# Kernel optimization log

Measured on AMD Instinct MI355X. Metric: run time of the kernel, lower is better.

Reference implementation:

```python
import jax, jax.numpy as jnp
import numpy as np

BN_EPS = 1e-5

def _square_distance(src, dst):
    # src [B,N,3], dst [B,S,3] -> [B,N,S]
    d = -2.0 * jnp.einsum('bnc,bsc->bns', src, dst)
    d = d + jnp.sum(src * src, -1)[:, :, None]
    d = d + jnp.sum(dst * dst, -1)[:, None, :]
    return d

def _conv_bn_relu(x, w, b, g, beta):
    # x [B,C,N]; 1x1 conv == channel GEMM, then training-mode batchnorm over (B,N)
    y = jnp.einsum('oc,bcn->bon', w, x) + b[None, :, None]
    mean = jnp.mean(y, axis=(0, 2), keepdims=True)
    var = jnp.mean((y - mean) ** 2, axis=(0, 2), keepdims=True)  # biased, as torch BN uses for normalization
    y = (y - mean) * jax.lax.rsqrt(var + BN_EPS)
    y = y * g[None, :, None] + beta[None, :, None]
    return jax.nn.relu(y)

def setup_inputs() -> dict:
    key = jax.random.key(0)
    ks = jax.random.split(key, 8)
    B, N, S, D1, D2 = 8, 8192, 2048, 128, 256
    C_in, C_mid, C_out = D1 + D2, 256, 256
    return {
        'xyz1': jax.random.normal(ks[0], (B, 3, N), jnp.float32),
        'xyz2': jax.random.normal(ks[1], (B, 3, S), jnp.float32),
        'points1': jax.random.normal(ks[2], (B, D1, N), jnp.float32),
        'points2': jax.random.normal(ks[3], (B, D2, S), jnp.float32),
        'w1': jax.random.normal(ks[4], (C_mid, C_in), jnp.float32) * (1.0 / np.sqrt(C_in)),
        'b1': jax.random.normal(ks[5], (C_mid,), jnp.float32) * 0.01,
        'g1': jnp.ones((C_mid,), jnp.float32),
        'beta1': jnp.zeros((C_mid,), jnp.float32),
        'w2': jax.random.normal(ks[6], (C_out, C_mid), jnp.float32) * (1.0 / np.sqrt(C_mid)),
        'b2': jax.random.normal(ks[7], (C_out,), jnp.float32) * 0.01,
        'g2': jnp.ones((C_out,), jnp.float32),
        'beta2': jnp.zeros((C_out,), jnp.float32),
    }

def reference(xyz1, xyz2, points1, points2, w1, b1, g1, beta1, w2, b2, g2, beta2):
    B = xyz1.shape[0]
    p1xyz = jnp.transpose(xyz1, (0, 2, 1))      # [B,N,3]
    p2xyz = jnp.transpose(xyz2, (0, 2, 1))      # [B,S,3]
    p2 = jnp.transpose(points2, (0, 2, 1))      # [B,S,D2]

    dists = _square_distance(p1xyz, p2xyz)      # [B,N,S]
    neg_d3, idx = jax.lax.top_k(-dists, 3)      # 3 smallest distances
    d3 = -neg_d3                                # [B,N,3]
    recip = 1.0 / (d3 + 1e-8)
    weight = recip / jnp.sum(recip, axis=2, keepdims=True)  # [B,N,3]

    gathered = jax.vmap(lambda p, i: p[i])(p2, idx)          # [B,N,3,D2]
    interp = jnp.sum(gathered * weight[..., None], axis=2)   # [B,N,D2]

    new_points = jnp.concatenate([jnp.transpose(points1, (0, 2, 1)), interp], axis=-1)
    x = jnp.transpose(new_points, (0, 2, 1))    # [B,D1+D2,N]
    x = _conv_bn_relu(x, w1, b1, g1, beta1)
    x = _conv_bn_relu(x, w2, b2, g2, beta2)
    return x
```

## Files before the change

### kernel.cpp

```cpp
#include <hip/hip_runtime.h>

#define B_    8
#define N_    8192
#define S_    2048
#define D1_   128
#define D2_   256
#define CIN_  384
#define CMID_ 256
#define COUT_ 256

typedef unsigned int  u32;
typedef unsigned short u16;
typedef __attribute__((ext_vector_type(8))) short short8;
typedef __attribute__((ext_vector_type(4))) float f32x4;

static __device__ __forceinline__ u32 uminu(u32 a, u32 b) { return a < b ? a : b; }
static __device__ __forceinline__ u32 umaxu(u32 a, u32 b) { return a > b ? a : b; }
static __device__ __forceinline__ u32 umed3(u32 a, u32 b, u32 c) {
  return umaxu(uminu(a, b), uminu(umaxu(a, b), c));
}
static __device__ __forceinline__ u16 f2bf(float f) {
  union { float f; u32 u; } v; v.f = f;
  u32 r = v.u + 0x7FFFu + ((v.u >> 16) & 1u);
  return (u16)(r >> 16);
}
static __device__ __forceinline__ float bflo(u32 u) { return __uint_as_float(u << 16); }
static __device__ __forceinline__ float bfhi(u32 u) { return __uint_as_float(u & 0xFFFF0000u); }

#define GLD16(g, l)                                                             \
  __builtin_amdgcn_global_load_lds((const __attribute__((address_space(1))) void*)(g), \
                                   (__attribute__((address_space(3))) void*)(l), 16, 0, 0)

__global__ __launch_bounds__(256) void k_prep(const float* __restrict__ xyz2,
                                              float4* __restrict__ pts4) {
  const int b = blockIdx.y, s = blockIdx.x * 256 + threadIdx.x;
  const float* xb = xyz2 + (size_t)b * 3 * S_;
  float x = xb[s], y = xb[S_ + s], z = xb[2 * S_ + s];
  pts4[b * S_ + s] = make_float4(-2.f * x, -2.f * y, -2.f * z, x * x + y * y + z * z);
}

__global__ __launch_bounds__(256) void k_nn_scan(const float* __restrict__ xyz1,
                                                 const float4* __restrict__ pts4,
                                                 uint4* __restrict__ keys) {
  const int b = blockIdx.z, chunk = blockIdx.y;
  const int n = blockIdx.x * 256 + threadIdx.x;
  const float* pb = xyz1 + (size_t)b * 3 * N_;
  const float px = pb[n], py = pb[N_ + n], pz = pb[2 * N_ + n];
  const float pn = px * px + py * py + pz * pz;
  const float4* __restrict__ P = pts4 + b * S_ + chunk * 512;
  const u32 sbase = chunk * 512;
  u32 m0 = ~0u, m1 = ~0u, m2 = ~0u, m3 = ~0u;
#pragma unroll 8
  for (int s = 0; s < 512; ++s) {
    float4 q = P[s];
    float d = fmaf(px, q.x, fmaf(py, q.y, fmaf(pz, q.z, pn + q.w)));
    d = fmaxf(d, 0.f);
    u32 k = (__float_as_uint(d) & 0xFFFFF800u) | (sbase + (u32)s);
    m3 = uminu(m3, umaxu(m2, k));
    m2 = umed3(m1, m2, k);
    m1 = umed3(m0, m1, k);
    m0 = uminu(m0, k);
  }
  uint4 v; v.x = m0; v.y = m1; v.z = m2; v.w = m3;
  keys[((size_t)(b * 4 + chunk)) * N_ + n] = v;
}

__global__ __launch_bounds__(256) void k_refine(const float* __restrict__ xyz1,
                                                const float4* __restrict__ pts4,
                                                const uint4* __restrict__ keys,
                                                int4* __restrict__ idx4,
                                                float4* __restrict__ w4) {
  const int b = blockIdx.y, n = blockIdx.x * 256 + threadIdx.x;
  const float* pb = xyz1 + (size_t)b * 3 * N_;
  const double px = (double)pb[n], py = (double)pb[N_ + n], pz = (double)pb[2 * N_ + n];
  const double pn = px * px + py * py + pz * pz;
  double bd0 = 1e300, bd1 = 1e300, bd2 = 1e300;
  int bi0 = 1 << 30, bi1 = 1 << 30, bi2 = 1 << 30;
#pragma unroll
  for (int c = 0; c < 4; ++c) {
    uint4 kk = keys[((size_t)(b * 4 + c)) * N_ + n];
    u32 arr[4] = {kk.x, kk.y, kk.z, kk.w};
#pragma unroll
    for (int j = 0; j < 4; ++j) {
      int s = (int)(arr[j] & 2047u);
      float4 q = pts4[b * S_ + s];
      double x = (double)(q.x * -0.5f), y = (double)(q.y * -0.5f), z = (double)(q.z * -0.5f);
      double dot = px * x + py * y + pz * z;
      double d = -2.0 * dot + (pn + (x * x + y * y + z * z));
      if (d < bd2 || (d == bd2 && s < bi2)) {
        if (d < bd1 || (d == bd1 && s < bi1)) {
          bd2 = bd1; bi2 = bi1;
          if (d < bd0 || (d == bd0 && s < bi0)) { bd1 = bd0; bi1 = bi0; bd0 = d; bi0 = s; }
          else                                  { bd1 = d;  bi1 = s; }
        } else { bd2 = d; bi2 = s; }
      }
    }
  }
  float f0 = (float)bd0, f1 = (float)bd1, f2 = (float)bd2;
  float r0 = 1.f / (f0 + 1e-8f), r1 = 1.f / (f1 + 1e-8f), r2 = 1.f / (f2 + 1e-8f);
  float rs = r0 + r1 + r2;
  w4[(size_t)b * N_ + n]   = make_float4(r0 / rs, r1 / rs, r2 / rs, 0.f);
  idx4[(size_t)b * N_ + n] = make_int4(bi0, bi1, bi2, 0);
}

__global__ __launch_bounds__(256) void k_p2t(const float* __restrict__ p2,
                                             float* __restrict__ p2T) {
  __shared__ float t[32][33];
  const int b = blockIdx.z, s0 = blockIdx.x * 32, d0 = blockIdx.y * 32;
  const int cc = threadIdx.x & 31, rr = threadIdx.x >> 5;
#pragma unroll
  for (int i = 0; i < 4; ++i) {
    int r = rr + i * 8;
    t[r][cc] = p2[((size_t)b * D2_ + d0 + r) * S_ + s0 + cc];
  }
  __syncthreads();
#pragma unroll
  for (int i = 0; i < 4; ++i) {
    int r = rr + i * 8;
    p2T[((size_t)b * S_ + s0 + r) * D2_ + d0 + cc] = t[cc][r];
  }
}

__global__ __launch_bounds__(256) void k_packp1(const float* __restrict__ p1,
                                                u16* __restrict__ xT) {
  __shared__ float t[32][33];
  const int b = blockIdx.z, n0 = blockIdx.x * 32, c0 = blockIdx.y * 32;
  const int cc = threadIdx.x & 31, rr = threadIdx.x >> 5;
#pragma unroll
  for (int i = 0; i < 4; ++i) {
    int r = rr + i * 8;
    t[r][cc] = p1[((size_t)b * D1_ + c0 + r) * N_ + n0 + cc];
  }
  __syncthreads();
#pragma unroll
  for (int i = 0; i < 4; ++i) {
    int r = rr + i * 8;
    xT[((size_t)b * N_ + n0 + r) * CIN_ + c0 + cc] = f2bf(t[cc][r]);
  }
}

__global__ __launch_bounds__(256) void k_gather_pack(const float* __restrict__ p2T,
                                                     const int4* __restrict__ idx4,
                                                     const float4* __restrict__ w4,
                                                     u16* __restrict__ xT) {
  const int b = blockIdx.y;
  const int wv = threadIdx.x >> 6, lane = threadIdx.x & 63;
  const int nbase = blockIdx.x * 16 + wv * 4;
  int4   id[4];
  float4 w[4];
#pragma unroll
  for (int i = 0; i < 4; ++i) {
    id[i] = idx4[(size_t)b * N_ + nbase + i];
    w[i]  = w4[(size_t)b * N_ + nbase + i];
  }
#pragma unroll
  for (int i = 0; i < 4; ++i) {
    const int n = nbase + i;
    const float4* r0 = (const float4*)(p2T + ((size_t)b * S_ + id[i].x) * D2_) + lane;
    const float4* r1 = (const float4*)(p2T + ((size_t)b * S_ + id[i].y) * D2_) + lane;
    const float4* r2 = (const float4*)(p2T + ((size_t)b * S_ + id[i].z) * D2_) + lane;
    float4 a = *r0, bb = *r1, cq = *r2;
    ushort4 pk;
    pk.x = f2bf(a.x * w[i].x + bb.x * w[i].y + cq.x * w[i].z);
    pk.y = f2bf(a.y * w[i].x + bb.y * w[i].y + cq.y * w[i].z);
    pk.z = f2bf(a.z * w[i].x + bb.z * w[i].y + cq.z * w[i].z);
    pk.w = f2bf(a.w * w[i].x + bb.w * w[i].y + cq.w * w[i].z);
    *(ushort4*)(xT + ((size_t)b * N_ + n) * CIN_ + D1_ + lane * 4) = pk;
  }
}

__global__ __launch_bounds__(256) void k_wcvt(const float* __restrict__ w1,
                                              const float* __restrict__ w2,
                                              u16* __restrict__ w1b,
                                              u16* __restrict__ w2b) {
  int i = blockIdx.x * 256 + threadIdx.x;
  if (i < CMID_ * CIN_) w1b[i] = f2bf(w1[i]);
  int j = i - CMID_ * CIN_;
  if (j >= 0 && j < COUT_ * CMID_) w2b[j] = f2bf(w2[j]);
}

__global__ __launch_bounds__(256) void k_gemm1(const u16* __restrict__ Wb,
                                               const float* __restrict__ bias,
                                               const u16* __restrict__ xT,
                                               u16* __restrict__ y1T) {
  __shared__ u16 As[128 * 32];
  __shared__ u16 Bs[128 * 32];
  const int b = blockIdx.z, bm0 = blockIdx.y * 128, bn0 = blockIdx.x * 128;
  const int tid = threadIdx.x, w = tid >> 6, l = tid & 63;
  const int wm = w & 1, wn = w >> 1;
  const int lr = l >> 2, lc = l & 3;
  const int fm = l & 15, fq = l >> 4;
  f32x4 acc[4][4];
#pragma unroll
  for (int i = 0; i < 4; ++i)
#pragma unroll
    for (int j = 0; j < 4; ++j) acc[i][j] = (f32x4){0.f, 0.f, 0.f, 0.f};

  for (int k0 = 0; k0 < CIN_; k0 += 32) {
    __syncthreads();
#pragma unroll
    for (int j = 0; j < 2; ++j) {
      int seg = w * 2 + j;
      int row = seg * 16 + lr;
      const u16* ga = Wb + (size_t)(bm0 + row) * CIN_ + k0 + lc * 8;
      const u16* gb = xT + ((size_t)b * N_ + bn0 + row) * CIN_ + k0 + lc * 8;
      GLD16(ga, &As[seg * 512]);
      GLD16(gb, &Bs[seg * 512]);
    }
    __syncthreads();
    short8 af[4], bfr[4];
#pragma unroll
    for (int f = 0; f < 4; ++f) {
      af[f]  = *(const short8*)&As[(wm * 64 + f * 16 + fm) * 32 + fq * 8];
      bfr[f] = *(const short8*)&Bs[(wn * 64 + f * 16 + fm) * 32 + fq * 8];
    }
#pragma unroll
    for (int i = 0; i < 4; ++i)
#pragma unroll
      for (int j = 0; j < 4; ++j)
        acc[i][j] = __builtin_amdgcn_mfma_f32_16x16x32_bf16(af[i], bfr[j], acc[i][j], 0, 0, 0);
  }
#pragma unroll
  for (int i = 0; i < 4; ++i) {
    int ob = bm0 + wm * 64 + i * 16 + fq * 4;
    float4 b4 = *(const float4*)(bias + ob);
#pragma unroll
    for (int j = 0; j < 4; ++j) {
      int n = bn0 + wn * 64 + j * 16 + fm;
      ushort4 pk;
      pk.x = f2bf(acc[i][j][0] + b4.x);
      pk.y = f2bf(acc[i][j][1] + b4.y);
      pk.z = f2bf(acc[i][j][2] + b4.z);
      pk.w = f2bf(acc[i][j][3] + b4.w);
      *(ushort4*)(y1T + ((size_t)b * N_ + n) * CMID_ + ob) = pk;
    }
  }
}

__global__ __launch_bounds__(256) void k_stats1(const u16* __restrict__ y1T,
                                                float* __restrict__ sum,
                                                float* __restrict__ sumsq) {
  __shared__ float ls[256], lss[256];
  const int b = blockIdx.y, chunk = blockIdx.x, tid = threadIdx.x;
  ls[tid] = 0.f; lss[tid] = 0.f;
  __syncthreads();
  const int c4 = (tid & 63) * 4, noff = tid >> 6;
  float s0 = 0, s1 = 0, s2 = 0, s3 = 0, q0 = 0, q1 = 0, q2 = 0, q3 = 0;
  for (int i = 0; i < 64; ++i) {
    int n = chunk * 256 + i * 4 + noff;
    ushort4 v = *(const ushort4*)(y1T + ((size_t)b * N_ + n) * CMID_ + c4);
    float f0 = __uint_as_float(((u32)v.x) << 16);
    float f1 = __uint_as_float(((u32)v.y) << 16);
    float f2 = __uint_as_float(((u32)v.z) << 16);
    float f3 = __uint_as_float(((u32)v.w) << 16);
    s0 += f0; s1 += f1; s2 += f2; s3 += f3;
    q0 += f0 * f0; q1 += f1 * f1; q2 += f2 * f2; q3 += f3 * f3;
  }
  atomicAdd(&ls[c4 + 0], s0); atomicAdd(&ls[c4 + 1], s1);
  atomicAdd(&ls[c4 + 2], s2); atomicAdd(&ls[c4 + 3], s3);
  atomicAdd(&lss[c4 + 0], q0); atomicAdd(&lss[c4 + 1], q1);
  atomicAdd(&lss[c4 + 2], q2); atomicAdd(&lss[c4 + 3], q3);
  __syncthreads();
  atomicAdd(&sum[tid], ls[tid]);
  atomicAdd(&sumsq[tid], lss[tid]);
}

__global__ __launch_bounds__(256) void k_affine(const float* __restrict__ sum,
                                                const float* __restrict__ sumsq,
                                                const float* __restrict__ g,
                                                const float* __restrict__ beta,
                                                float* __restrict__ scale,
                                                float* __restrict__ shift) {
  int o = threadIdx.x;
  const float inv = 1.0f / (float)(B_ * N_);
  float m = sum[o] * inv;
  float var = sumsq[o] * inv - m * m;
  float sc = g[o] / sqrtf(var + 1e-5f);
  scale[o] = sc;
  shift[o] = beta[o] - m * sc;
}

__global__ __launch_bounds__(256) void k_gemm2(const u16* __restrict__ Wb2,
                                               const float* __restrict__ b2,
                                               const u16* __restrict__ y1T,
                                               const float* __restrict__ scale,
                                               const float* __restrict__ shift,
                                               float* __restrict__ out) {
  __shared__ u16 As[128 * 32];
  __shared__ u16 Bs[128 * 32];
  const int b = blockIdx.z, bm0 = blockIdx.y * 128, bn0 = blockIdx.x * 128;
  const int tid = threadIdx.x, w = tid >> 6, l = tid & 63;
  const int wm = w & 1, wn = w >> 1;
  const int lr = l >> 2, lc = l & 3;
  const int fm = l & 15, fq = l >> 4;
  f32x4 acc[4][4];
#pragma unroll
  for (int i = 0; i < 4; ++i)
#pragma unroll
    for (int j = 0; j < 4; ++j) acc[i][j] = (f32x4){0.f, 0.f, 0.f, 0.f};

  for (int k0 = 0; k0 < CMID_; k0 += 32) {
    __syncthreads();
#pragma unroll
    for (int j = 0; j < 2; ++j) {
      int seg = w * 2 + j;
      int row = seg * 16 + lr;
      const u16* ga = Wb2 + (size_t)(bm0 + row) * CMID_ + k0 + lc * 8;
      GLD16(ga, &As[seg * 512]);
    }
#pragma unroll
    for (int i = 0; i < 2; ++i) {
      int li = tid + i * 256;
      int n = li >> 2, cp = li & 3;
      int c = k0 + cp * 8;
      uint4 r = *(const uint4*)(y1T + ((size_t)b * N_ + bn0 + n) * CMID_ + c);
      float4 sA = *(const float4*)(scale + c);
      float4 sB = *(const float4*)(scale + c + 4);
      float4 hA = *(const float4*)(shift + c);
      float4 hB = *(const float4*)(shift + c + 4);
      float v0 = fmaxf(fmaf(bflo(r.x), sA.x, hA.x), 0.f);
      float v1 = fmaxf(fmaf(bfhi(r.x), sA.y, hA.y), 0.f);
      float v2 = fmaxf(fmaf(bflo(r.y), sA.z, hA.z), 0.f);
      float v3 = fmaxf(fmaf(bfhi(r.y), sA.w, hA.w), 0.f);
      float v4 = fmaxf(fmaf(bflo(r.z), sB.x, hB.x), 0.f);
      float v5 = fmaxf(fmaf(bfhi(r.z), sB.y, hB.y), 0.f);
      float v6 = fmaxf(fmaf(bflo(r.w), sB.z, hB.z), 0.f);
      float v7 = fmaxf(fmaf(bfhi(r.w), sB.w, hB.w), 0.f);
      uint4 pk;
      pk.x = (u32)f2bf(v0) | ((u32)f2bf(v1) << 16);
      pk.y = (u32)f2bf(v2) | ((u32)f2bf(v3) << 16);
      pk.z = (u32)f2bf(v4) | ((u32)f2bf(v5) << 16);
      pk.w = (u32)f2bf(v6) | ((u32)f2bf(v7) << 16);
      *(uint4*)&Bs[n * 32 + cp * 8] = pk;
    }
    __syncthreads();
    short8 af[4], bfr[4];
#pragma unroll
    for (int f = 0; f < 4; ++f) {
      af[f]  = *(const short8*)&As[(wm * 64 + f * 16 + fm) * 32 + fq * 8];
      bfr[f] = *(const short8*)&Bs[(wn * 64 + f * 16 + fm) * 32 + fq * 8];
    }
#pragma unroll
    for (int i = 0; i < 4; ++i)
#pragma unroll
      for (int j = 0; j < 4; ++j)
        acc[i][j] = __builtin_amdgcn_mfma_f32_16x16x32_bf16(af[i], bfr[j], acc[i][j], 0, 0, 0);
  }
#pragma unroll
  for (int i = 0; i < 4; ++i) {
    int ob = bm0 + wm * 64 + i * 16 + fq * 4;
    float4 b4 = *(const float4*)(b2 + ob);
#pragma unroll
    for (int j = 0; j < 4; ++j) {
      int n = bn0 + wn * 64 + j * 16 + fm;
      out[((size_t)b * COUT_ + ob + 0) * N_ + n] = acc[i][j][0] + b4.x;
      out[((size_t)b * COUT_ + ob + 1) * N_ + n] = acc[i][j][1] + b4.y;
      out[((size_t)b * COUT_ + ob + 2) * N_ + n] = acc[i][j][2] + b4.z;
      out[((size_t)b * COUT_ + ob + 3) * N_ + n] = acc[i][j][3] + b4.w;
    }
  }
}

__global__ __launch_bounds__(256) void k_stats(const float* __restrict__ y,
                                               float* __restrict__ sum,
                                               float* __restrict__ sumsq) {
  const int o = blockIdx.x, b = blockIdx.y;
  const float4* row = (const float4*)(y + ((size_t)b * 256 + o) * N_);
  float s = 0.f, ss = 0.f;
  for (int i = threadIdx.x; i < N_ / 4; i += 256) {
    float4 v = row[i];
    s  += v.x + v.y + v.z + v.w;
    ss += v.x * v.x + v.y * v.y + v.z * v.z + v.w * v.w;
  }
  for (int off = 32; off; off >>= 1) {
    s  += __shfl_down(s, off);
    ss += __shfl_down(ss, off);
  }
  __shared__ float red[8];
  int w = threadIdx.x >> 6, lane = threadIdx.x & 63;
  if (lane == 0) { red[w] = s; red[4 + w] = ss; }
  __syncthreads();
  if (threadIdx.x == 0) {
    float S  = red[0] + red[1] + red[2] + red[3];
    float SS = red[4] + red[5] + red[6] + red[7];
    atomicAdd(&sum[o], S);
    atomicAdd(&sumsq[o], SS);
  }
}

__global__ __launch_bounds__(256) void k_bn2(float* __restrict__ y,
                                             const float* __restrict__ scale,
                                             const float* __restrict__ shift) {
  const int o = blockIdx.x, b = blockIdx.y;
  float sc = scale[o], sh = shift[o];
  float4* row = (float4*)(y + ((size_t)b * COUT_ + o) * N_);
  for (int i = threadIdx.x; i < N_ / 4; i += 256) {
    float4 v = row[i];
    v.x = fmaxf(fmaf(v.x, sc, sh), 0.f);
    v.y = fmaxf(fmaf(v.y, sc, sh), 0.f);
    v.z = fmaxf(fmaf(v.z, sc, sh), 0.f);
    v.w = fmaxf(fmaf(v.w, sc, sh), 0.f);
    row[i] = v;
  }
}

extern "C" void kernel_launch(void* const* d_in, const int* in_sizes, int n_in,
                              void* d_out, int out_size, void* d_ws, size_t ws_size,
                              hipStream_t stream) {
  const float* xyz1    = (const float*)d_in[0];
  const float* xyz2    = (const float*)d_in[1];
  const float* points1 = (const float*)d_in[2];
  const float* points2 = (const float*)d_in[3];
  const float* w1      = (const float*)d_in[4];
  const float* b1      = (const float*)d_in[5];
  const float* g1      = (const float*)d_in[6];
  const float* beta1   = (const float*)d_in[7];
  const float* w2      = (const float*)d_in[8];
  const float* b2      = (const float*)d_in[9];
  const float* g2      = (const float*)d_in[10];
  const float* beta2   = (const float*)d_in[11];
  float* out = (float*)d_out;

  char* ws = (char*)d_ws;
  size_t off = 0;
  u16*    xT    = (u16*)(ws + off);   off += (size_t)B_ * N_ * CIN_ * 2;
  u16*    y1T   = (u16*)(ws + off);   off += (size_t)B_ * N_ * CMID_ * 2;
  float*  p2T   = (float*)(ws + off); off += (size_t)B_ * S_ * D2_ * 4;
  float4* pts4  = (float4*)(ws + off); off += (size_t)B_ * S_ * 16;
  uint4*  keys  = (uint4*)(ws + off); off += (size_t)B_ * 4 * N_ * 16;
  int4*   idx4  = (int4*)(ws + off);  off += (size_t)B_ * N_ * 16;
  float4* w4    = (float4*)(ws + off); off += (size_t)B_ * N_ * 16;
  u16*    w1b   = (u16*)(ws + off);   off += (size_t)CMID_ * CIN_ * 2;
  u16*    w2b   = (u16*)(ws + off);   off += (size_t)COUT_ * CMID_ * 2;
  float*  stats = (float*)(ws + off);

  hipMemsetAsync(stats, 0, 1024 * sizeof(float), stream);

  k_wcvt       <<<dim3((CMID_ * CIN_ + COUT_ * CMID_) / 256), 256, 0, stream>>>(w1, w2, w1b, w2b);
  k_prep       <<<dim3(S_ / 256, B_), 256, 0, stream>>>(xyz2, pts4);
  k_p2t        <<<dim3(S_ / 32, D2_ / 32, B_), 256, 0, stream>>>(points2, p2T);
  k_nn_scan    <<<dim3(N_ / 256, 4, B_), 256, 0, stream>>>(xyz1, pts4, keys);
  k_refine     <<<dim3(N_ / 256, B_), 256, 0, stream>>>(xyz1, pts4, keys, idx4, w4);
  k_packp1     <<<dim3(N_ / 32, D1_ / 32, B_), 256, 0, stream>>>(points1, xT);
  k_gather_pack<<<dim3(N_ / 16, B_), 256, 0, stream>>>(p2T, idx4, w4, xT);
  k_gemm1      <<<dim3(N_ / 128, CMID_ / 128, B_), 256, 0, stream>>>(w1b, b1, xT, y1T);
  k_stats1     <<<dim3(N_ / 256, B_), 256, 0, stream>>>(y1T, stats + 0, stats + 256);
  k_affine     <<<1, 256, 0, stream>>>(stats + 0, stats + 256, g1, beta1, stats + 1024, stats + 1280);
  k_gemm2      <<<dim3(N_ / 128, COUT_ / 128, B_), 256, 0, stream>>>(w2b, b2, y1T, stats + 1024, stats + 1280, out);
  k_stats      <<<dim3(COUT_, B_), 256, 0, stream>>>(out, stats + 512, stats + 768);
  k_affine     <<<1, 256, 0, stream>>>(stats + 512, stats + 768, g2, beta2, stats + 1536, stats + 1792);
  k_bn2        <<<dim3(COUT_, B_), 256, 0, stream>>>(out, stats + 1536, stats + 1792);
}
```

Measured before the change: 309.0 us.

## Fuse BN statistics into GEMM epilogues, store bf16 y2, split NN scan finer

Computes batchnorm sum and sum-of-squares inside the epilogues of both GEMMs with shared-memory atomics, removing the separate stats kernels and their re-read of the activations. GEMM2 now writes a bf16 transposed intermediate that reuses the xT buffer, and a new tiled kernel applies the BN affine and ReLU while transposing into the fp32 output, replacing the old full fp32 read-modify-write pass. The nearest-neighbour scan is split into 8 chunks of 256 points instead of 4 of 512, which doubles parallelism and keeps more distance mantissa bits in the packed key, at the cost of twice as many candidates to refine. Rounding the layer-2 output to bf16 before normalisation adds precision error.

```diff
diff --git a/kernel.cpp b/kernel.cpp
--- a/kernel.cpp
+++ b/kernel.cpp
@@ -47,22 +47,21 @@
   const float* pb = xyz1 + (size_t)b * 3 * N_;
   const float px = pb[n], py = pb[N_ + n], pz = pb[2 * N_ + n];
   const float pn = px * px + py * py + pz * pz;
-  const float4* __restrict__ P = pts4 + b * S_ + chunk * 512;
-  const u32 sbase = chunk * 512;
+  const float4* __restrict__ P = pts4 + b * S_ + chunk * 256;
   u32 m0 = ~0u, m1 = ~0u, m2 = ~0u, m3 = ~0u;
 #pragma unroll 8
-  for (int s = 0; s < 512; ++s) {
+  for (int s = 0; s < 256; ++s) {
     float4 q = P[s];
     float d = fmaf(px, q.x, fmaf(py, q.y, fmaf(pz, q.z, pn + q.w)));
     d = fmaxf(d, 0.f);
-    u32 k = (__float_as_uint(d) & 0xFFFFF800u) | (sbase + (u32)s);
+    u32 k = (__float_as_uint(d) & 0xFFFFFF00u) | (u32)s;
     m3 = uminu(m3, umaxu(m2, k));
     m2 = umed3(m1, m2, k);
     m1 = umed3(m0, m1, k);
     m0 = uminu(m0, k);
   }
   uint4 v; v.x = m0; v.y = m1; v.z = m2; v.w = m3;
-  keys[((size_t)(b * 4 + chunk)) * N_ + n] = v;
+  keys[((size_t)(b * 8 + chunk)) * N_ + n] = v;
 }
 
 __global__ __launch_bounds__(256) void k_refine(const float* __restrict__ xyz1,
@@ -77,12 +76,12 @@
   double bd0 = 1e300, bd1 = 1e300, bd2 = 1e300;
   int bi0 = 1 << 30, bi1 = 1 << 30, bi2 = 1 << 30;
 #pragma unroll
-  for (int c = 0; c < 4; ++c) {
-    uint4 kk = keys[((size_t)(b * 4 + c)) * N_ + n];
+  for (int c = 0; c < 8; ++c) {
+    uint4 kk = keys[((size_t)(b * 8 + c)) * N_ + n];
     u32 arr[4] = {kk.x, kk.y, kk.z, kk.w};
 #pragma unroll
     for (int j = 0; j < 4; ++j) {
-      int s = (int)(arr[j] & 2047u);
+      int s = c * 256 + (int)(arr[j] & 255u);
       float4 q = pts4[b * S_ + s];
       double x = (double)(q.x * -0.5f), y = (double)(q.y * -0.5f), z = (double)(q.z * -0.5f);
       double dot = px * x + py * y + pz * z;
@@ -182,14 +181,18 @@
 __global__ __launch_bounds__(256) void k_gemm1(const u16* __restrict__ Wb,
                                                const float* __restrict__ bias,
                                                const u16* __restrict__ xT,
-                                               u16* __restrict__ y1T) {
+                                               u16* __restrict__ y1T,
+                                               float* __restrict__ sum,
+                                               float* __restrict__ sumsq) {
   __shared__ u16 As[128 * 32];
   __shared__ u16 Bs[128 * 32];
+  __shared__ float s_sum[128], s_ssq[128];
   const int b = blockIdx.z, bm0 = blockIdx.y * 128, bn0 = blockIdx.x * 128;
   const int tid = threadIdx.x, w = tid >> 6, l = tid & 63;
   const int wm = w & 1, wn = w >> 1;
   const int lr = l >> 2, lc = l & 3;
   const int fm = l & 15, fq = l >> 4;
+  if (tid < 128) { s_sum[tid] = 0.f; s_ssq[tid] = 0.f; }
   f32x4 acc[4][4];
 #pragma unroll
   for (int i = 0; i < 4; ++i)
@@ -224,6 +227,7 @@
   for (int i = 0; i < 4; ++i) {
     int ob = bm0 + wm * 64 + i * 16 + fq * 4;
     float4 b4 = *(const float4*)(bias + ob);
+    float sv0 = 0, sv1 = 0, sv2 = 0, sv3 = 0, qv0 = 0, qv1 = 0, qv2 = 0, qv3 = 0;
 #pragma unroll
     for (int j = 0; j < 4; ++j) {
       int n = bn0 + wn * 64 + j * 16 + fm;
@@ -233,36 +237,22 @@
       pk.z = f2bf(acc[i][j][2] + b4.z);
       pk.w = f2bf(acc[i][j][3] + b4.w);
       *(ushort4*)(y1T + ((size_t)b * N_ + n) * CMID_ + ob) = pk;
-    }
-  }
-}
-
-__global__ __launch_bounds__(256) void k_stats1(const u16* __restrict__ y1T,
-                                                float* __restrict__ sum,
-                                                float* __restrict__ sumsq) {
-  __shared__ float ls[256], lss[256];
-  const int b = blockIdx.y, chunk = blockIdx.x, tid = threadIdx.x;
-  ls[tid] = 0.f; lss[tid] = 0.f;
+      float v0 = bflo(pk.x), v1 = bflo(pk.y), v2 = bflo(pk.z), v3 = bflo(pk.w);
+      sv0 += v0; sv1 += v1; sv2 += v2; sv3 += v3;
+      qv0 = fmaf(v0, v0, qv0); qv1 = fmaf(v1, v1, qv1);
+      qv2 = fmaf(v2, v2, qv2); qv3 = fmaf(v3, v3, qv3);
+    }
+    int ol = wm * 64 + i * 16 + fq * 4;
+    atomicAdd(&s_sum[ol + 0], sv0); atomicAdd(&s_sum[ol + 1], sv1);
+    atomicAdd(&s_sum[ol + 2], sv2); atomicAdd(&s_sum[ol + 3], sv3);
+    atomicAdd(&s_ssq[ol + 0], qv0); atomicAdd(&s_ssq[ol + 1], qv1);
+    atomicAdd(&s_ssq[ol + 2], qv2); atomicAdd(&s_ssq[ol + 3], qv3);
+  }
   __syncthreads();
-  const int c4 = (tid & 63) * 4, noff = tid >> 6;
-  float s0 = 0, s1 = 0, s2 = 0, s3 = 0, q0 = 0, q1 = 0, q2 = 0, q3 = 0;
-  for (int i = 0; i < 64; ++i) {
-    int n = chunk * 256 + i * 4 + noff;
-    ushort4 v = *(const ushort4*)(y1T + ((size_t)b * N_ + n) * CMID_ + c4);
-    float f0 = __uint_as_float(((u32)v.x) << 16);
-    float f1 = __uint_as_float(((u32)v.y) << 16);
-    float f2 = __uint_as_float(((u32)v.z) << 16);
-    float f3 = __uint_as_float(((u32)v.w) << 16);
-    s0 += f0; s1 += f1; s2 += f2; s3 += f3;
-    q0 += f0 * f0; q1 += f1 * f1; q2 += f2 * f2; q3 += f3 * f3;
-  }
-  atomicAdd(&ls[c4 + 0], s0); atomicAdd(&ls[c4 + 1], s1);
-  atomicAdd(&ls[c4 + 2], s2); atomicAdd(&ls[c4 + 3], s3);
-  atomicAdd(&lss[c4 + 0], q0); atomicAdd(&lss[c4 + 1], q1);
-  atomicAdd(&lss[c4 + 2], q2); atomicAdd(&lss[c4 + 3], q3);
-  __syncthreads();
-  atomicAdd(&sum[tid], ls[tid]);
-  atomicAdd(&sumsq[tid], lss[tid]);
+  if (tid < 128) {
+    atomicAdd(&sum[bm0 + tid], s_sum[tid]);
+    atomicAdd(&sumsq[bm0 + tid], s_ssq[tid]);
+  }
 }
 
 __global__ __launch_bounds__(256) void k_affine(const float* __restrict__ sum,
@@ -285,14 +275,18 @@
                                                const u16* __restrict__ y1T,
                                                const float* __restrict__ scale,
                                                const float* __restrict__ shift,
-                                               float* __restrict__ out) {
+                                               u16* __restrict__ y2T,
+                                               float* __restrict__ sum,
+                                               float* __restrict__ sumsq) {
   __shared__ u16 As[128 * 32];
   __shared__ u16 Bs[128 * 32];
+  __shared__ float s_sum[128], s_ssq[128];
   const int b = blockIdx.z, bm0 = blockIdx.y * 128, bn0 = blockIdx.x * 128;
   const int tid = threadIdx.x, w = tid >> 6, l = tid & 63;
   const int wm = w & 1, wn = w >> 1;
   const int lr = l >> 2, lc = l & 3;
   const int fm = l & 15, fq = l >> 4;
+  if (tid < 128) { s_sum[tid] = 0.f; s_ssq[tid] = 0.f; }
   f32x4 acc[4][4];
 #pragma unroll
   for (int i = 0; i < 4; ++i)
@@ -350,57 +344,53 @@
   for (int i = 0; i < 4; ++i) {
     int ob = bm0 + wm * 64 + i * 16 + fq * 4;
     float4 b4 = *(const float4*)(b2 + ob);
+    float sv0 = 0, sv1 = 0, sv2 = 0, sv3 = 0, qv0 = 0, qv1 = 0, qv2 = 0, qv3 = 0;
 #pragma unroll
     for (int j = 0; j < 4; ++j) {
       int n = bn0 + wn * 64 + j * 16 + fm;
-      out[((size_t)b * COUT_ + ob + 0) * N_ + n] = acc[i][j][0] + b4.x;
-      out[((size_t)b * COUT_ + ob + 1) * N_ + n] = acc[i][j][1] + b4.y;
-      out[((size_t)b * COUT_ + ob + 2) * N_ + n] = acc[i][j][2] + b4.z;
-      out[((size_t)b * COUT_ + ob + 3) * N_ + n] = acc[i][j][3] + b4.w;
-    }
-  }
-}
-
-__global__ __launch_bounds__(256) void k_stats(const float* __restrict__ y,
-                                               float* __restrict__ sum,
-                                               float* __restrict__ sumsq) {
-  const int o = blockIdx.x, b = blockIdx.y;
-  const float4* row = (const float4*)(y + ((size_t)b * 256 + o) * N_);
-  float s = 0.f, ss = 0.f;
-  for (int i = threadIdx.x; i < N_ / 4; i += 256) {
-    float4 v = row[i];
-    s  += v.x + v.y + v.z + v.w;
-    ss += v.x * v.x + v.y * v.y + v.z * v.z + v.w * v.w;
-  }
-  for (int off = 32; off; off >>= 1) {
-    s  += __shfl_down(s, off);
-    ss += __shfl_down(ss, off);
-  }
-  __shared__ float red[8];
-  int w = threadIdx.x >> 6, lane = threadIdx.x & 63;
-  if (lane == 0) { red[w] = s; red[4 + w] = ss; }
+      ushort4 pk;
+      pk.x = f2bf(acc[i][j][0] + b4.x);
+      pk.y = f2bf(acc[i][j][1] + b4.y);
+      pk.z = f2bf(acc[i][j][2] + b4.z);
+      pk.w = f2bf(acc[i][j][3] + b4.w);
+      *(ushort4*)(y2T + ((size_t)b * N_ + n) * COUT_ + ob) = pk;
+      float v0 = bflo(pk.x), v1 = bflo(pk.y), v2 = bflo(pk.z), v3 = bflo(pk.w);
+      sv0 += v0; sv1 += v1; sv2 += v2; sv3 += v3;
+      qv0 = fmaf(v0, v0, qv0); qv1 = fmaf(v1, v1, qv1);
+      qv2 = fmaf(v2, v2, qv2); qv3 = fmaf(v3, v3, qv3);
+    }
+    int ol = wm * 64 + i * 16 + fq * 4;
+    atomicAdd(&s_sum[ol + 0], sv0); atomicAdd(&s_sum[ol + 1], sv1);
+    atomicAdd(&s_sum[ol + 2], sv2); atomicAdd(&s_sum[ol + 3], sv3);
+    atomicAdd(&s_ssq[ol + 0], qv0); atomicAdd(&s_ssq[ol + 1], qv1);
+    atomicAdd(&s_ssq[ol + 2], qv2); atomicAdd(&s_ssq[ol + 3], qv3);
+  }
   __syncthreads();
-  if (threadIdx.x == 0) {
-    float S  = red[0] + red[1] + red[2] + red[3];
-    float SS = red[4] + red[5] + red[6] + red[7];
-    atomicAdd(&sum[o], S);
-    atomicAdd(&sumsq[o], SS);
-  }
-}
-
-__global__ __launch_bounds__(256) void k_bn2(float* __restrict__ y,
-                                             const float* __restrict__ scale,
-                                             const float* __restrict__ shift) {
-  const int o = blockIdx.x, b = blockIdx.y;
-  float sc = scale[o], sh = shift[o];
-  float4* row = (float4*)(y + ((size_t)b * COUT_ + o) * N_);
-  for (int i = threadIdx.x; i < N_ / 4; i += 256) {
-    float4 v = row[i];
-    v.x = fmaxf(fmaf(v.x, sc, sh), 0.f);
-    v.y = fmaxf(fmaf(v.y, sc, sh), 0.f);
-    v.z = fmaxf(fmaf(v.z, sc, sh), 0.f);
-    v.w = fmaxf(fmaf(v.w, sc, sh), 0.f);
-    row[i] = v;
+  if (tid < 128) {
+    atomicAdd(&sum[bm0 + tid], s_sum[tid]);
+    atomicAdd(&sumsq[bm0 + tid], s_ssq[tid]);
+  }
+}
+
+__global__ __launch_bounds__(256) void k_bn2t(const u16* __restrict__ y2T,
+                                              const float* __restrict__ scale,
+                                              const float* __restrict__ shift,
+                                              float* __restrict__ out) {
+  __shared__ float t[32][33];
+  const int b = blockIdx.z, n0 = blockIdx.x * 32, o0 = blockIdx.y * 32;
+  const int cc = threadIdx.x & 31, rr = threadIdx.x >> 5;
+  const float sc = scale[o0 + cc], sh = shift[o0 + cc];
+#pragma unroll
+  for (int i = 0; i < 4; ++i) {
+    int r = rr + i * 8;
+    float v = bflo((u32)y2T[((size_t)b * N_ + n0 + r) * COUT_ + o0 + cc]);
+    t[r][cc] = fmaxf(fmaf(v, sc, sh), 0.f);
+  }
+  __syncthreads();
+#pragma unroll
+  for (int i = 0; i < 4; ++i) {
+    int r = rr + i * 8;
+    out[((size_t)b * COUT_ + o0 + r) * N_ + n0 + cc] = t[cc][r];
   }
 }
 
@@ -423,31 +413,33 @@
 
   char* ws = (char*)d_ws;
   size_t off = 0;
-  u16*    xT    = (u16*)(ws + off);   off += (size_t)B_ * N_ * CIN_ * 2;
-  u16*    y1T   = (u16*)(ws + off);   off += (size_t)B_ * N_ * CMID_ * 2;
-  float*  p2T   = (float*)(ws + off); off += (size_t)B_ * S_ * D2_ * 4;
+  u16*    xT    = (u16*)(ws + off);    off += (size_t)B_ * N_ * CIN_ * 2;
+  u16*    y1T   = (u16*)(ws + off);    off += (size_t)B_ * N_ * CMID_ * 2;
+  float*  p2T   = (float*)(ws + off);  off += (size_t)B_ * S_ * D2_ * 4;
   float4* pts4  = (float4*)(ws + off); off += (size_t)B_ * S_ * 16;
-  uint4*  keys  = (uint4*)(ws + off); off += (size_t)B_ * 4 * N_ * 16;
-  int4*   idx4  = (int4*)(ws + off);  off += (size_t)B_ * N_ * 16;
+  uint4*  keys  = (uint4*)(ws + off);  off += (size_t)B_ * 8 * N_ * 16;
+  int4*   idx4  = (int4*)(ws + off);   off += (size_t)B_ * N_ * 16;
   float4* w4    = (float4*)(ws + off); off += (size_t)B_ * N_ * 16;
-  u16*    w1b   = (u16*)(ws + off);   off += (size_t)CMID_ * CIN_ * 2;
-  u16*    w2b   = (u16*)(ws + off);   off += (size_t)COUT_ * CMID_ * 2;
+  u16*    w1b   = (u16*)(ws + off);    off += (size_t)CMID_ * CIN_ * 2;
+  u16*    w2b   = (u16*)(ws + off);    off += (size_t)COUT_ * CMID_ * 2;
   float*  stats = (float*)(ws + off);
+  u16*    y2T   = xT;
 
   hipMemsetAsync(stats, 0, 1024 * sizeof(float), stream);
 
   k_wcvt       <<<dim3((CMID_ * CIN_ + COUT_ * CMID_) / 256), 256, 0, stream>>>(w1, w2, w1b, w2b);
   k_prep       <<<dim3(S_ / 256, B_), 256, 0, stream>>>(xyz2, pts4);
   k_p2t        <<<dim3(S_ / 32, D2_ / 32, B_), 256, 0, stream>>>(points2, p2T);
-  k_nn_scan    <<<dim3(N_ / 256, 4, B_), 256, 0, stream>>>(xyz1, pts4, keys);
+  k_nn_scan    <<<dim3(N_ / 256, 8, B_), 256, 0, stream>>>(xyz1, pts4, keys);
   k_refine     <<<dim3(N_ / 256, B_), 256, 0, stream>>>(xyz1, pts4, keys, idx4, w4);
   k_packp1     <<<dim3(N_ / 32, D1_ / 32, B_), 256, 0, stream>>>(points1, xT);
   k_gather_pack<<<dim3(N_ / 16, B_), 256, 0, stream>>>(p2T, idx4, w4, xT);
-  k_gemm1      <<<dim3(N_ / 128, CMID_ / 128, B_), 256, 0, stream>>>(w1b, b1, xT, y1T);
-  k_stats1     <<<dim3(N_ / 256, B_), 256, 0, stream>>>(y1T, stats + 0, stats + 256);
+  k_gemm1      <<<dim3(N_ / 128, CMID_ / 128, B_), 256, 0, stream>>>(w1b, b1, xT, y1T,
+                                                                     stats + 0, stats + 256);
   k_affine     <<<1, 256, 0, stream>>>(stats + 0, stats + 256, g1, beta1, stats + 1024, stats + 1280);
-  k_gemm2      <<<dim3(N_ / 128, COUT_ / 128, B_), 256, 0, stream>>>(w2b, b2, y1T, stats + 1024, stats + 1280, out);
-  k_stats      <<<dim3(COUT_, B_), 256, 0, stream>>>(out, stats + 512, stats + 768);
+  k_gemm2      <<<dim3(N_ / 128, COUT_ / 128, B_), 256, 0, stream>>>(w2b, b2, y1T,
+                                                                     stats + 1024, stats + 1280,
+                                                                     y2T, stats + 512, stats + 768);
   k_affine     <<<1, 256, 0, stream>>>(stats + 512, stats + 768, g2, beta2, stats + 1536, stats + 1792);
-  k_bn2        <<<dim3(COUT_, B_), 256, 0, stream>>>(out, stats + 1536, stats + 1792);
-}
+  k_bn2t       <<<dim3(N_ / 32, COUT_ / 32, B_), 256, 0, stream>>>(y2T, stats + 1536, stats + 1792, out);
+}
```

After: 380.5 us. 1.23x slower.
